# Optimization experiments

Measured on AMD Instinct MI355X. Metric: run time of the kernel, lower is better.

## Reference

```python
import jax, jax.numpy as jnp
import numpy as np

B, S, FEAT, HID, H = 8, 1024, 1024, 1024, 8
DH = HID // H  # head dim = 128
MASK_VAL = -128.0  # mask_val = -2**7 (soft additive mask, per original code)


def setup_inputs() -> dict:
    key = jax.random.key(0)
    ks = jax.random.split(key, 4)
    scale = 0.02
    return {
        "queries": jax.random.normal(ks[0], (B, S, FEAT), dtype=jnp.float32),
        "Wq": jax.random.normal(ks[1], (FEAT, HID), dtype=jnp.float32) * scale,
        "bq": jnp.zeros((HID,), dtype=jnp.float32),
        "Wk": jax.random.normal(ks[2], (FEAT, HID), dtype=jnp.float32) * scale,
        "bk": jnp.zeros((HID,), dtype=jnp.float32),
        "Wv": jax.random.normal(ks[3], (FEAT, HID), dtype=jnp.float32) * scale,
        "bv": jnp.zeros((HID,), dtype=jnp.float32),
    }


def reference(queries, Wq, bq, Wk, bk, Wv, bv):
    # Self-attention: keys = values = queries (torch forward defaults)
    q = queries @ Wq + bq  # [B,S,HID]
    k = queries @ Wk + bk
    v = queries @ Wv + bv
    # split heads: chunk along last dim == reshape (B,S,H,DH)
    qh = q.reshape(B, S, H, DH)
    kh = k.reshape(B, S, H, DH)
    vh = v.reshape(B, S, H, DH)
    # exp-scaled-dot score (non-standard: exp BEFORE mask/softmax)
    logits = jnp.einsum("bqhd,bkhd->bhqk", qh, kh) / np.float32(np.sqrt(DH))
    score = jnp.exp(logits)
    # soft additive causal mask: upper triangle (diag=1) gets -128
    mask = jnp.triu(jnp.full((S, S), MASK_VAL, dtype=score.dtype), k=1)
    att = jax.nn.softmax(score + mask, axis=-1)  # [B,H,S,S]
    ctx = jnp.einsum("bhqk,bkhd->bqhd", att, vh)  # [B,S,H,DH]
    # reverse heads: concat along last dim
    return ctx.reshape(B, S, HID)
```

## Files before the change

### kernel.cpp

```cpp
#include <hip/hip_runtime.h>


typedef __bf16 bf16x8 __attribute__((ext_vector_type(8)));
typedef float floatx4 __attribute__((ext_vector_type(4)));
typedef unsigned int u32x4 __attribute__((ext_vector_type(4)));
typedef unsigned long long u64;
typedef u64 u64x2 __attribute__((ext_vector_type(2)));
typedef unsigned short u16;
typedef unsigned int u32;

#define LOG2E 1.4426950408889634f
#define QSCALE 0.12751743f
#define PSEL 0x07060302u

__device__ __forceinline__ u32 pkbf16(float lo, float hi) {
  return __builtin_amdgcn_perm(__float_as_uint(hi) + 0x8000u,
                               __float_as_uint(lo) + 0x8000u, PSEL);
}
__device__ __forceinline__ u16 b16(float f) {
  return (u16)((__float_as_uint(f) + 0x8000u) >> 16);
}

__device__ __forceinline__ void gld_lds16(const void* g, void* l) {
  __builtin_amdgcn_global_load_lds(
      (const __attribute__((address_space(1))) unsigned*)g,
      (__attribute__((address_space(3))) unsigned*)l, 16, 0, 0);
}

#define MFMA16(a, b, c) __builtin_amdgcn_mfma_f32_16x16x32_bf16(a, b, c, 0, 0, 0)

__global__ __launch_bounds__(256) void prep_kernel(
    const float4* __restrict__ X, u16* __restrict__ Xb,
    const float* __restrict__ Wq, const float* __restrict__ Wk,
    const float* __restrict__ Wv, u16* __restrict__ Wtb) {
  if (blockIdx.x < 8192) {
    unsigned i = blockIdx.x * 256u + threadIdx.x;
    float4 v = X[i];
    uint2 o;
    o.x = pkbf16(v.x, v.y);
    o.y = pkbf16(v.z, v.w);
    *reinterpret_cast<uint2*>(Xb + 4u * i) = o;
  } else {
    const int bid = blockIdx.x - 8192;
    const int mat = bid >> 10;
    const int bx = bid & 31, by = (bid >> 5) & 31;
    const float* W = (mat == 0) ? Wq : (mat == 1) ? Wk : Wv;
    const float ws = (mat == 0) ? QSCALE : 1.0f;
    u16* Wt = Wtb + (size_t)mat * (1024u * 1024u);
    __shared__ u16 tile[32][33];
    const int x = threadIdx.x & 31, y = threadIdx.x >> 5;
    const int kt = bx * 32, nt = by * 32;
#pragma unroll
    for (int i = 0; i < 4; ++i)
      tile[y + 8 * i][x] = b16(W[(size_t)(kt + y + 8 * i) * 1024 + nt + x] * ws);
    __syncthreads();
#pragma unroll
    for (int i = 0; i < 4; ++i)
      Wt[(size_t)(nt + y + 8 * i) * 1024 + kt + x] = tile[x][y + 8 * i];
  }
}

__global__ __launch_bounds__(256, 2) void gemm_qkv_kernel(
    const u16* __restrict__ Xb, const u16* __restrict__ Wtb,
    const float* __restrict__ bq, const float* __restrict__ bk,
    const float* __restrict__ bv, u16* __restrict__ Qh, u16* __restrict__ Kh,
    u16* __restrict__ Vt) {
  const int mat = blockIdx.z;
  const u16* __restrict__ Wt = Wtb + (size_t)mat * (1024u * 1024u);
  const float* __restrict__ bias = (mat == 0) ? bq : (mat == 1) ? bk : bv;
  const float bscale = (mat == 0) ? QSCALE : 1.0f;

  const int m0 = blockIdx.x * 128;
  const int n0 = blockIdx.y * 128;

  __shared__ u16 As[2][128 * 64];
  __shared__ u16 Bs[2][128 * 64];

  const int tid = threadIdx.x;
  const int wid = tid >> 6;
  const int lane = tid & 63;
  const int quad = lane >> 4;
  const int l16 = lane & 15;
  const int wm = (wid & 1) * 64;
  const int wn = (wid >> 1) * 64;

  const floatx4 z4 = {0.f, 0.f, 0.f, 0.f};
  floatx4 acc[4][4];
#pragma unroll
  for (int i = 0; i < 4; ++i)
#pragma unroll
    for (int j = 0; j < 4; ++j) acc[i][j] = z4;

  const int srow = wid * 32;
  const int lrow = lane >> 3;
  const int gblk = (lane & 7) ^ lrow;

  auto stage = [&](int b, int k0) {
#pragma unroll
    for (int c = 0; c < 4; ++c) {
      const int row = srow + c * 8 + lrow;
      gld_lds16(Xb + (size_t)(m0 + row) * 1024 + k0 + gblk * 8,
                As[b] + (srow + c * 8) * 64);
      gld_lds16(Wt + (size_t)(n0 + row) * 1024 + k0 + gblk * 8,
                Bs[b] + (srow + c * 8) * 64);
    }
  };

  stage(0, 0);

  for (int i = 0; i < 16; ++i) {
    __syncthreads();
    if (i < 15) stage((i + 1) & 1, (i + 1) * 64);

    const u16* __restrict__ Ab = As[i & 1];
    const u16* __restrict__ Bb = Bs[i & 1];
#pragma unroll
    for (int c = 0; c < 2; ++c) {
      const int phys = ((c * 4 + quad) ^ (l16 & 7)) * 8;
      bf16x8 af[4], bfr[4];
#pragma unroll
      for (int ii = 0; ii < 4; ++ii)
        af[ii] = *(const bf16x8*)(Ab + (wm + ii * 16 + l16) * 64 + phys);
#pragma unroll
      for (int j = 0; j < 4; ++j)
        bfr[j] = *(const bf16x8*)(Bb + (wn + j * 16 + l16) * 64 + phys);
#pragma unroll
      for (int ii = 0; ii < 4; ++ii)
#pragma unroll
        for (int j = 0; j < 4; ++j)
          acc[ii][j] = MFMA16(af[ii], bfr[j], acc[ii][j]);
    }
  }

  const int b = m0 >> 10;
  const int h = n0 >> 7;
  const int sbase = (m0 & 1023) + wm;
  float bv4[4];
#pragma unroll
  for (int j = 0; j < 4; ++j) bv4[j] = bias[n0 + wn + j * 16 + l16] * bscale;

  if (mat < 2) {
    u16* outp = (mat == 0 ? Qh : Kh) + (size_t)(b * 8 + h) * 1024 * 128;
#pragma unroll
    for (int i = 0; i < 4; ++i)
#pragma unroll
      for (int j = 0; j < 4; ++j) {
        const int d = wn + j * 16 + l16;
#pragma unroll
        for (int r = 0; r < 4; ++r) {
          const int s = sbase + i * 16 + quad * 4 + r;
          outp[(size_t)s * 128 + d] = b16(acc[i][j][r] + bv4[j]);
        }
      }
  } else {
    u16* outp = Vt + (size_t)(b * 8 + h) * 128 * 1024;
#pragma unroll
    for (int i = 0; i < 4; ++i)
#pragma unroll
      for (int j = 0; j < 4; ++j) {
        const int d = wn + j * 16 + l16;
        const int s = sbase + i * 16 + quad * 4;
        uint2 pk;
        pk.x = pkbf16(acc[i][j][0] + bv4[j], acc[i][j][1] + bv4[j]);
        pk.y = pkbf16(acc[i][j][2] + bv4[j], acc[i][j][3] + bv4[j]);
        *(uint2*)(outp + (size_t)d * 1024 + s) = pk;
      }
  }
}

__global__ __launch_bounds__(256, 2) void attn_kernel(const u16* __restrict__ Qh,
                                                      const u16* __restrict__ Kh,
                                                      const u16* __restrict__ Vt,
                                                      float* __restrict__ out) {
  const int id = blockIdx.x;
  const int bh = (id & 7) * 8 + ((id >> 3) & 7);
  const int QTMAP[8] = {7, 4, 6, 5, 0, 3, 1, 2};
  const int qt = QTMAP[id >> 6];
  const int q0 = qt * 128;

  const int tid = threadIdx.x;
  const int wid = tid >> 6;
  const int lane = tid & 63;
  const int quad = lane >> 4;
  const int l16 = lane & 15;

  __shared__ u16 Ks[2][32 * 128];
  __shared__ u16 Vs[2][128 * 32];

  const u16* __restrict__ Qbase = Qh + (size_t)bh * 1024 * 128;
  const u16* __restrict__ Kbase = Kh + (size_t)bh * 1024 * 128;
  const u16* __restrict__ Vbase = Vt + (size_t)bh * 128 * 1024;

  const int qw = q0 + wid * 32;

  bf16x8 qf[2][4];
#pragma unroll
  for (int nt = 0; nt < 2; ++nt)
#pragma unroll
    for (int c = 0; c < 4; ++c)
      qf[nt][c] = *(const bf16x8*)(Qbase + (size_t)(qw + nt * 16 + l16) * 128 +
                                   c * 32 + quad * 8);

  const floatx4 z4 = {0.f, 0.f, 0.f, 0.f};
  floatx4 o[2][8];
#pragma unroll
  for (int nt = 0; nt < 2; ++nt)
#pragma unroll
    for (int dt = 0; dt < 8; ++dt) o[nt][dt] = z4;
  float lacc[2] = {0.f, 0.f};

  auto stage = [&](int b, int k0) {
#pragma unroll
    for (int c = 0; c < 2; ++c) {
      const int r0 = wid * 8 + c * 4;
      const int row = r0 + quad;
      gld_lds16(Kbase + (size_t)(k0 + row) * 128 + ((l16 ^ (row & 15)) * 8),
                Ks[b] + r0 * 128);
    }
#pragma unroll
    for (int c = 0; c < 2; ++c) {
      const int r0 = wid * 32 + c * 16;
      const int row = r0 + (lane >> 2);
      gld_lds16(Vbase + (size_t)row * 1024 + k0 + (lane & 3) * 8,
                Vs[b] + r0 * 32);
    }
  };

  const int n = (q0 + 128) >> 5;
  stage(0, 0);

  for (int i = 0; i < n; ++i) {
    const int k0 = i << 5;
    __syncthreads();
    if (i + 1 < n) stage((i + 1) & 1, k0 + 32);

    if (k0 <= qw + 31) {
      const u16* __restrict__ Kb = Ks[i & 1];
      const u16* __restrict__ Vb = Vs[i & 1];
      const bool diag = (k0 == qw);

      u32 pw[2][4];
#pragma unroll
      for (int f = 0; f < 2; ++f) {
        bf16x8 kf[4];
#pragma unroll
        for (int c = 0; c < 4; ++c)
          kf[c] = *(const bf16x8*)(Kb + (f * 16 + l16) * 128 +
                                   (((c * 4 + quad) ^ l16) * 8));
        floatx4 st[2];
#pragma unroll
        for (int nt = 0; nt < 2; ++nt) {
          st[nt] = z4;
#pragma unroll
          for (int c = 0; c < 4; ++c) st[nt] = MFMA16(kf[c], qf[nt][c], st[nt]);
        }
#pragma unroll
        for (int nt = 0; nt < 2; ++nt) {
          float p[4];
#pragma unroll
          for (int r = 0; r < 4; ++r) {
            const float e = fminf(__builtin_amdgcn_exp2f(st[nt][r]), 85.f);
            p[r] = __builtin_amdgcn_exp2f(e * LOG2E);
          }
          if (diag) {
#pragma unroll
            for (int r = 0; r < 4; ++r)
              p[r] = (f * 16 + quad * 4 + r > nt * 16 + l16) ? 0.f : p[r];
          }
          lacc[nt] += (p[0] + p[1]) + (p[2] + p[3]);
          pw[nt][f * 2 + 0] = pkbf16(p[0], p[1]);
          pw[nt][f * 2 + 1] = pkbf16(p[2], p[3]);
        }
      }

      bf16x8 pa[2];
#pragma unroll
      for (int nt = 0; nt < 2; ++nt) {
        u32x4 t;
        t.x = pw[nt][0]; t.y = pw[nt][1]; t.z = pw[nt][2]; t.w = pw[nt][3];
        pa[nt] = __builtin_bit_cast(bf16x8, t);
      }
#pragma unroll
      for (int dt = 0; dt < 8; ++dt) {
        const int d = dt * 16 + l16;
        u64x2 t;
        t.x = *(const u64*)(Vb + d * 32 + quad * 4);
        t.y = *(const u64*)(Vb + d * 32 + 16 + quad * 4);
        const bf16x8 vf = __builtin_bit_cast(bf16x8, t);
        o[0][dt] = MFMA16(vf, pa[0], o[0][dt]);
        o[1][dt] = MFMA16(vf, pa[1], o[1][dt]);
      }
    }
  }

  float linv[2];
#pragma unroll
  for (int nt = 0; nt < 2; ++nt) {
    float s = lacc[nt];
    s += __shfl_xor(s, 16);
    s += __shfl_xor(s, 32);
    linv[nt] = 1.0f / s;
  }

  float* outp = out + (size_t)(bh >> 3) * 1024 * 1024 + (bh & 7) * 128;
#pragma unroll
  for (int nt = 0; nt < 2; ++nt) {
    const int qrow = qw + nt * 16 + l16;
#pragma unroll
    for (int dt = 0; dt < 8; ++dt) {
      float4 v;
      v.x = o[nt][dt][0] * linv[nt];
      v.y = o[nt][dt][1] * linv[nt];
      v.z = o[nt][dt][2] * linv[nt];
      v.w = o[nt][dt][3] * linv[nt];
      *(float4*)(outp + (size_t)qrow * 1024 + dt * 16 + quad * 4) = v;
    }
  }
}

extern "C" void kernel_launch(void* const* d_in, const int* in_sizes, int n_in,
                              void* d_out, int out_size, void* d_ws,
                              size_t ws_size, hipStream_t stream) {
  const float* X = (const float*)d_in[0];
  const float* Wq = (const float*)d_in[1];
  const float* bq = (const float*)d_in[2];
  const float* Wk = (const float*)d_in[3];
  const float* bk = (const float*)d_in[4];
  const float* Wv = (const float*)d_in[5];
  const float* bv = (const float*)d_in[6];
  float* out = (float*)d_out;

  char* ws = (char*)d_ws;
  u16* Xb  = (u16*)(ws);
  u16* Wtb = (u16*)(ws + (16u << 20));
  u16* Qh  = (u16*)(ws + (22u << 20));
  u16* Kh  = (u16*)(ws + (38u << 20));
  u16* Vt  = (u16*)(ws + (54u << 20));

  prep_kernel<<<8192 + 3072, 256, 0, stream>>>((const float4*)X, Xb, Wq, Wk,
                                               Wv, Wtb);
  dim3 gg(64, 8, 3);
  gemm_qkv_kernel<<<gg, 256, 0, stream>>>(Xb, Wtb, bq, bk, bv, Qh, Kh, Vt);
  attn_kernel<<<512, 256, 0, stream>>>(Qh, Kh, Vt, out);
}
```

Baseline: 220.1 us.

## Pair mirrored query tiles per block to balance causal work and swizzle V LDS

Each attention block now handles two 64-row query chunks, one from the front and one mirrored from the back of the sequence. This makes the causal work per block roughly equal and replaces the fixed tile-order map used before. It also XOR-swizzles the V tile layout in LDS to cut bank conflicts on the V fragment reads. The cost is more per-block bookkeeping (active flags and per-chunk diagonal masking), and each block now loops up to the later chunk's diagonal.

```diff
diff --git a/kernel.cpp b/kernel.cpp
--- a/kernel.cpp
+++ b/kernel.cpp
@@ -174,9 +174,9 @@
                                                       float* __restrict__ out) {
   const int id = blockIdx.x;
   const int bh = (id & 7) * 8 + ((id >> 3) & 7);
-  const int QTMAP[8] = {7, 4, 6, 5, 0, 3, 1, 2};
-  const int qt = QTMAP[id >> 6];
-  const int q0 = qt * 128;
+  const int pi = id >> 6;
+  const int qa = pi * 64;
+  const int qb = (15 - pi) * 64;
 
   const int tid = threadIdx.x;
   const int wid = tid >> 6;
@@ -191,22 +191,22 @@
   const u16* __restrict__ Kbase = Kh + (size_t)bh * 1024 * 128;
   const u16* __restrict__ Vbase = Vt + (size_t)bh * 128 * 1024;
 
-  const int qw = q0 + wid * 32;
+  const int rP[2] = {qa + wid * 16 + l16, qb + wid * 16 + l16};
 
   bf16x8 qf[2][4];
 #pragma unroll
-  for (int nt = 0; nt < 2; ++nt)
+  for (int P = 0; P < 2; ++P)
 #pragma unroll
     for (int c = 0; c < 4; ++c)
-      qf[nt][c] = *(const bf16x8*)(Qbase + (size_t)(qw + nt * 16 + l16) * 128 +
-                                   c * 32 + quad * 8);
+      qf[P][c] = *(const bf16x8*)(Qbase + (size_t)rP[P] * 128 + c * 32 +
+                                  quad * 8);
 
   const floatx4 z4 = {0.f, 0.f, 0.f, 0.f};
   floatx4 o[2][8];
 #pragma unroll
-  for (int nt = 0; nt < 2; ++nt)
-#pragma unroll
-    for (int dt = 0; dt < 8; ++dt) o[nt][dt] = z4;
+  for (int P = 0; P < 2; ++P)
+#pragma unroll
+    for (int dt = 0; dt < 8; ++dt) o[P][dt] = z4;
   float lacc[2] = {0.f, 0.f};
 
   auto stage = [&](int b, int k0) {
@@ -221,99 +221,102 @@
     for (int c = 0; c < 2; ++c) {
       const int r0 = wid * 32 + c * 16;
       const int row = r0 + (lane >> 2);
-      gld_lds16(Vbase + (size_t)row * 1024 + k0 + (lane & 3) * 8,
-                Vs[b] + r0 * 32);
+      const int gu = (lane & 3) ^ ((row >> 1) & 3);
+      gld_lds16(Vbase + (size_t)row * 1024 + k0 + gu * 8, Vs[b] + r0 * 32);
     }
   };
 
-  const int n = (q0 + 128) >> 5;
+  const int kd[2] = {qa + (wid >> 1) * 32, qb + (wid >> 1) * 32};
+  const int nB = (qb + 64) >> 5;
+
+  const int e4 = (l16 >> 1) & 3;
+  const int sx = (((((quad >> 1) ^ e4) << 1) | (quad & 1))) * 4;
+  const int sy = ((((2 + (quad >> 1)) ^ e4) << 1) | (quad & 1)) * 4;
+
   stage(0, 0);
 
-  for (int i = 0; i < n; ++i) {
+  for (int i = 0; i < nB; ++i) {
     const int k0 = i << 5;
     __syncthreads();
-    if (i + 1 < n) stage((i + 1) & 1, k0 + 32);
-
-    if (k0 <= qw + 31) {
-      const u16* __restrict__ Kb = Ks[i & 1];
-      const u16* __restrict__ Vb = Vs[i & 1];
-      const bool diag = (k0 == qw);
-
-      u32 pw[2][4];
-#pragma unroll
-      for (int f = 0; f < 2; ++f) {
-        bf16x8 kf[4];
-#pragma unroll
-        for (int c = 0; c < 4; ++c)
-          kf[c] = *(const bf16x8*)(Kb + (f * 16 + l16) * 128 +
-                                   (((c * 4 + quad) ^ l16) * 8));
-        floatx4 st[2];
-#pragma unroll
-        for (int nt = 0; nt < 2; ++nt) {
-          st[nt] = z4;
-#pragma unroll
-          for (int c = 0; c < 4; ++c) st[nt] = MFMA16(kf[c], qf[nt][c], st[nt]);
+    if (i + 1 < nB) stage((i + 1) & 1, k0 + 32);
+
+    const bool act[2] = {k0 <= kd[0], k0 <= kd[1]};
+    if (!act[0] && !act[1]) continue;
+
+    const u16* __restrict__ Kb = Ks[i & 1];
+    const u16* __restrict__ Vb = Vs[i & 1];
+
+    u32 pw[2][4];
+#pragma unroll
+    for (int f = 0; f < 2; ++f) {
+      bf16x8 kf[4];
+#pragma unroll
+      for (int c = 0; c < 4; ++c)
+        kf[c] = *(const bf16x8*)(Kb + (f * 16 + l16) * 128 +
+                                 (((c * 4 + quad) ^ l16) * 8));
+#pragma unroll
+      for (int P = 0; P < 2; ++P) {
+        if (!act[P]) continue;
+        const bool diag = (k0 == kd[P]);
+        if (diag && f == 1 && !(wid & 1)) {
+          pw[P][2] = 0u; pw[P][3] = 0u;
+          continue;
         }
-#pragma unroll
-        for (int nt = 0; nt < 2; ++nt) {
-          float p[4];
-#pragma unroll
-          for (int r = 0; r < 4; ++r) {
-            const float e = fminf(__builtin_amdgcn_exp2f(st[nt][r]), 85.f);
-            p[r] = __builtin_amdgcn_exp2f(e * LOG2E);
-          }
-          if (diag) {
-#pragma unroll
-            for (int r = 0; r < 4; ++r)
-              p[r] = (f * 16 + quad * 4 + r > nt * 16 + l16) ? 0.f : p[r];
-          }
-          lacc[nt] += (p[0] + p[1]) + (p[2] + p[3]);
-          pw[nt][f * 2 + 0] = pkbf16(p[0], p[1]);
-          pw[nt][f * 2 + 1] = pkbf16(p[2], p[3]);
+        floatx4 st = z4;
+#pragma unroll
+        for (int c = 0; c < 4; ++c) st = MFMA16(kf[c], qf[P][c], st);
+        float p[4];
+#pragma unroll
+        for (int r = 0; r < 4; ++r) {
+          const float e = fminf(__builtin_amdgcn_exp2f(st[r]), 85.f);
+          p[r] = __builtin_amdgcn_exp2f(e * LOG2E);
         }
+        if (diag && f == (wid & 1)) {
+#pragma unroll
+          for (int r = 0; r < 4; ++r)
+            p[r] = (quad * 4 + r > l16) ? 0.f : p[r];
+        }
+        lacc[P] += (p[0] + p[1]) + (p[2] + p[3]);
+        pw[P][f * 2 + 0] = pkbf16(p[0], p[1]);
+        pw[P][f * 2 + 1] = pkbf16(p[2], p[3]);
       }
-
-      bf16x8 pa[2];
-#pragma unroll
-      for (int nt = 0; nt < 2; ++nt) {
+    }
+
+    bf16x8 pa[2];
+#pragma unroll
+    for (int P = 0; P < 2; ++P)
+      if (act[P]) {
         u32x4 t;
-        t.x = pw[nt][0]; t.y = pw[nt][1]; t.z = pw[nt][2]; t.w = pw[nt][3];
-        pa[nt] = __builtin_bit_cast(bf16x8, t);
+        t.x = pw[P][0]; t.y = pw[P][1]; t.z = pw[P][2]; t.w = pw[P][3];
+        pa[P] = __builtin_bit_cast(bf16x8, t);
       }
 #pragma unroll
-      for (int dt = 0; dt < 8; ++dt) {
-        const int d = dt * 16 + l16;
-        u64x2 t;
-        t.x = *(const u64*)(Vb + d * 32 + quad * 4);
-        t.y = *(const u64*)(Vb + d * 32 + 16 + quad * 4);
-        const bf16x8 vf = __builtin_bit_cast(bf16x8, t);
-        o[0][dt] = MFMA16(vf, pa[0], o[0][dt]);
-        o[1][dt] = MFMA16(vf, pa[1], o[1][dt]);
-      }
-    }
-  }
-
-  float linv[2];
-#pragma unroll
-  for (int nt = 0; nt < 2; ++nt) {
-    float s = lacc[nt];
+    for (int dt = 0; dt < 8; ++dt) {
+      const int d = dt * 16 + l16;
+      u64x2 t;
+      t.x = *(const u64*)(Vb + d * 32 + sx);
+      t.y = *(const u64*)(Vb + d * 32 + sy);
+      const bf16x8 vf = __builtin_bit_cast(bf16x8, t);
+      if (act[0]) o[0][dt] = MFMA16(vf, pa[0], o[0][dt]);
+      if (act[1]) o[1][dt] = MFMA16(vf, pa[1], o[1][dt]);
+    }
+  }
+
+  float* outp = out + (size_t)(bh >> 3) * 1024 * 1024 + (bh & 7) * 128;
+#pragma unroll
+  for (int P = 0; P < 2; ++P) {
+    float s = lacc[P];
     s += __shfl_xor(s, 16);
     s += __shfl_xor(s, 32);
-    linv[nt] = 1.0f / s;
-  }
-
-  float* outp = out + (size_t)(bh >> 3) * 1024 * 1024 + (bh & 7) * 128;
-#pragma unroll
-  for (int nt = 0; nt < 2; ++nt) {
-    const int qrow = qw + nt * 16 + l16;
+    const float linv = 1.0f / s;
 #pragma unroll
     for (int dt = 0; dt < 8; ++dt) {
       float4 v;
-      v.x = o[nt][dt][0] * linv[nt];
-      v.y = o[nt][dt][1] * linv[nt];
-      v.z = o[nt][dt][2] * linv[nt];
-      v.w = o[nt][dt][3] * linv[nt];
-      *(float4*)(outp + (size_t)qrow * 1024 + dt * 16 + quad * 4) = v;
+      v.x = o[P][dt][0] * linv;
+      v.y = o[P][dt][1] * linv;
+      v.z = o[P][dt][2] * linv;
+      v.w = o[P][dt][3] * linv;
+      *(float4*)(outp + (size_t)rP[P] * 1024 + dt * 16 + quad * 4) = v;
     }
   }
 }
```

New measurement: 199.3 us. -9.5%, faster.
